# Kernel optimization log

Measured on AMD Instinct MI355X. Metric: run time of the kernel, lower is better.

Reference implementation:

```python
import jax, jax.numpy as jnp
import numpy as np

D_MODEL = 1024
D_STATE = 16
D_CONV = 4
EXPAND = 1
D_INNER = EXPAND * D_MODEL  # must equal D_MODEL for original dt_proj shapes to work
BATCH = 2
SEQ = 2048


def silu(x):
    return x * jax.nn.sigmoid(x)


def setup_inputs() -> dict:
    key = jax.random.key(0)
    ks = jax.random.split(key, 8)
    s = 0.02
    return {
        "x": jax.random.normal(ks[0], (BATCH, SEQ, D_MODEL), dtype=jnp.float32),
        "W_in": jax.random.normal(ks[1], (2 * D_INNER, D_MODEL), dtype=jnp.float32) * s,
        "conv_w": jax.random.normal(ks[2], (D_INNER, D_CONV), dtype=jnp.float32) * s,
        "conv_b": jnp.zeros((D_INNER,), dtype=jnp.float32),
        "W_dt": jax.random.normal(ks[3], (D_INNER, D_INNER), dtype=jnp.float32) * s,
        "b_dt": jnp.zeros((D_INNER,), dtype=jnp.float32),
        "A_log": jnp.zeros((D_INNER, D_STATE), dtype=jnp.float32),  # torch: log(ones)=0
        "Bp": jax.random.normal(ks[4], (D_INNER, D_STATE), dtype=jnp.float32),
        "Cp": jax.random.normal(ks[5], (D_INNER, D_STATE), dtype=jnp.float32),
        "Dp": jnp.ones((D_INNER,), dtype=jnp.float32),
        "W_out": jax.random.normal(ks[6], (D_MODEL, D_INNER), dtype=jnp.float32) * s,
    }


def reference(x, W_in, conv_w, conv_b, W_dt, b_dt, A_log, Bp, Cp, Dp, W_out):
    B, L, _ = x.shape
    # in_proj then split into ssm branch and gating residual
    xr = x @ W_in.T                               # (B, L, 2*D_INNER)
    x_proj, res = jnp.split(xr, 2, axis=-1)       # each (B, L, D_INNER)

    # causal depthwise conv1d (kernel D_CONV), == torch conv1d(padding=K-1)[..., :L]
    xp = jnp.pad(x_proj, ((0, 0), (D_CONV - 1, 0), (0, 0)))
    xc = conv_b + sum(conv_w[:, k] * xp[:, k:k + L, :] for k in range(D_CONV))
    xc = silu(xc)                                 # (B, L, D_INNER)

    # selective SSM scan
    delta = jax.nn.softplus(xc @ W_dt.T + b_dt)   # (B, L, D_INNER)
    A = -jnp.exp(A_log)                           # (D_INNER, D_STATE)
    dA = jnp.exp(delta[..., None] * A)            # (B, L, D_INNER, D_STATE)
    dBx = delta[..., None] * Bp * xc[..., None]   # (B, L, D_INNER, D_STATE)

    def step(h, inp):
        dA_t, dBx_t = inp                         # (B, D_INNER, D_STATE)
        h = dA_t * h + dBx_t
        y = jnp.einsum('bdn,dn->bd', h, Cp)
        return h, y

    h0 = jnp.zeros((B, D_INNER, D_STATE), dtype=x.dtype)
    _, ys = jax.lax.scan(step, h0, (dA.transpose(1, 0, 2, 3), dBx.transpose(1, 0, 2, 3)))
    x_ssm = ys.transpose(1, 0, 2) + xc * Dp       # (B, L, D_INNER)

    return (x_ssm * silu(res)) @ W_out.T          # (B, L, D_MODEL)
```

## Files before the change

### kernel.cpp

```cpp
#include <hip/hip_runtime.h>

typedef unsigned short u16;
typedef __bf16 bf16;
typedef bf16 bf16x8 __attribute__((ext_vector_type(8)));
typedef float f32x4 __attribute__((ext_vector_type(4)));

#define SEQ     2048
#define BATCH   2
#define DM      1024
#define DI      1024
#define NROW    (BATCH*SEQ)
#define NSTATE  16
#define NCHUNK  64
#define CLEN    32
#define BK      32

static_assert(SEQ == NCHUNK * CLEN, "chunking must cover SEQ");

__device__ __forceinline__ u16 f2bf(float f) {
  unsigned u = __builtin_bit_cast(unsigned, f);
  u += 0x7FFFu + ((u >> 16) & 1u);
  return (u16)(u >> 16);
}
__device__ __forceinline__ float sigm(float x) { return 1.f / (1.f + __expf(-x)); }

__global__ __launch_bounds__(256) void k_cvt_all(
    const float* __restrict__ x, const float* __restrict__ Win,
    const float* __restrict__ Wdt, const float* __restrict__ Wout,
    u16* __restrict__ xbf, u16* __restrict__ winbf,
    u16* __restrict__ wdtbf, u16* __restrict__ woutbf)
{
  long i = (long)blockIdx.x * 256 + threadIdx.x;
  const float* src; u16* dst; long off;
  if (i < 1048576)            { src = x;    dst = xbf;    off = i; }
  else if (i < 1572864)       { src = Win;  dst = winbf;  off = i - 1048576; }
  else if (i < 1835008)       { src = Wdt;  dst = wdtbf;  off = i - 1572864; }
  else                        { src = Wout; dst = woutbf; off = i - 1835008; }
  float4 v = reinterpret_cast<const float4*>(src)[off];
  ushort4 o;
  o.x = f2bf(v.x); o.y = f2bf(v.y); o.z = f2bf(v.z); o.w = f2bf(v.w);
  reinterpret_cast<ushort4*>(dst)[off] = o;
}


__device__ __forceinline__ void gload16(const u16* g, u16* l) {
  __builtin_amdgcn_global_load_lds((const __attribute__((address_space(1))) void*)g,
                                   (__attribute__((address_space(3))) void*)l,
                                   16, 0, 0);
}

template<int EPI, int BM, int BN, int GX>
__global__ __launch_bounds__(256, 4) void k_gemm(
    const u16* __restrict__ A, const u16* __restrict__ B,
    float* __restrict__ out0, float* __restrict__ out1,
    const float* __restrict__ bias, int M, int N, int K)
{
  constexpr int MI_ = BM / 32;
  constexpr int NI_ = BN / 32;
  __shared__ __align__(16) u16 sA[2 * BM * BK];
  __shared__ __align__(16) u16 sB[2 * BN * BK];
  const int t = threadIdx.x;
  const int wave = t >> 6, lane = t & 63;
  const int lr = lane & 15, kb = lane >> 4;
  const int wr = wave >> 1, wc = wave & 1;

  const int nwg = gridDim.x;
  const int bid = blockIdx.x;
  const int wg  = (bid & 7) * (nwg >> 3) + (bid >> 3);
  const long bm = (long)(wg / GX) * BM;
  const long bn = (long)(wg % GX) * BN;

  f32x4 acc[MI_][NI_] = {};

  const int srow = t >> 2;
  const int scol = (t & 3) * 8;
  const u16* gA0 = A + (bm + srow) * (long)K + scol;
  const u16* gB0 = B + (bn + srow) * (long)K + scol;

  auto STAGE = [&](int buf, int k0) {
    #pragma unroll
    for (int i = 0; i < BM / 64; ++i)
      gload16(gA0 + (long)i * 64 * K + k0,
              &sA[buf * (BM * BK) + i * (64 * BK) + wave * 512]);
    #pragma unroll
    for (int i = 0; i < BN / 64; ++i)
      gload16(gB0 + (long)i * 64 * K + k0,
              &sB[buf * (BN * BK) + i * (64 * BK) + wave * 512]);
  };

  STAGE(0, 0);
  __syncthreads();
  int cur = 0;
  for (int k0 = 0; k0 < K; k0 += BK) {
    if (k0 + BK < K) STAGE(cur ^ 1, k0 + BK);
    const u16* pa = &sA[cur * (BM * BK) + (wr * (BM / 2) + lr) * BK + kb * 8];
    const u16* pb = &sB[cur * (BN * BK) + (wc * (BN / 2) + lr) * BK + kb * 8];
    bf16x8 af[MI_], bfr[NI_];
    #pragma unroll
    for (int mi = 0; mi < MI_; ++mi)
      af[mi] = *reinterpret_cast<const bf16x8*>(pa + mi * 16 * BK);
    #pragma unroll
    for (int ni = 0; ni < NI_; ++ni)
      bfr[ni] = *reinterpret_cast<const bf16x8*>(pb + ni * 16 * BK);
    #pragma unroll
    for (int mi = 0; mi < MI_; ++mi)
      #pragma unroll
      for (int ni = 0; ni < NI_; ++ni)
        acc[mi][ni] = __builtin_amdgcn_mfma_f32_16x16x32_bf16(af[mi], bfr[ni], acc[mi][ni], 0, 0, 0);
    __syncthreads();
    cur ^= 1;
  }

  #pragma unroll
  for (int mi = 0; mi < MI_; ++mi) {
    const long row0 = bm + wr * (BM / 2) + mi * 16 + kb * 4;
    #pragma unroll
    for (int ni = 0; ni < NI_; ++ni) {
      const long col = bn + wc * (BN / 2) + ni * 16 + lr;
      #pragma unroll
      for (int j = 0; j < 4; ++j) {
        const float v = acc[mi][ni][j];
        const long r = row0 + j;
        if (EPI == 0) {
          out0[r * N + col] = v;
        } else if (EPI == 1) {
          if (col < DI) out0[r * DI + col] = v;
          else          out1[r * DI + (col - DI)] = v * sigm(v);
        } else {
          float z = v + bias[col];
          out0[r * N + col] = fmaxf(z, 0.f) + log1pf(__expf(-fabsf(z)));
        }
      }
    }
  }
}

__global__ void k_conv(const float* __restrict__ xproj, const float* __restrict__ convw,
                       const float* __restrict__ convb, float* __restrict__ xc,
                       u16* __restrict__ xcbf)
{
  const int idx = blockIdx.x * 256 + threadIdx.x;
  const int d = idx & (DI - 1);
  const int m = idx >> 10;
  const int l = m & (SEQ - 1);
  float acc = convb[d];
  #pragma unroll
  for (int k = 0; k < 4; ++k) {
    int ls = l + k - 3;
    if (ls >= 0)
      acc = fmaf(convw[d * 4 + k], xproj[(long)(m + k - 3) * DI + d], acc);
  }
  float s = acc * sigm(acc);
  xc[idx] = s;
  xcbf[idx] = f2bf(s);
}

__global__ __launch_bounds__(256) void k_scanA(
    const float* __restrict__ delta, const float* __restrict__ xc,
    const float* __restrict__ A_log, const float* __restrict__ Bp,
    float* __restrict__ hfin, float* __restrict__ sumdt_buf)
{
  const int tid = threadIdx.x, blk = blockIdx.x;
  const int d = (blk & 3) * 256 + tid;
  const int c = (blk >> 2) & (NCHUNK - 1);
  const int b = blk >> 8;
  float Aa[NSTATE], Bb[NSTATE], h[NSTATE];
  #pragma unroll
  for (int n = 0; n < NSTATE; ++n) {
    Aa[n] = -__expf(A_log[d * NSTATE + n]);
    Bb[n] = Bp[d * NSTATE + n];
    h[n] = 0.f;
  }
  const long base = ((long)(b * SEQ + c * CLEN)) * DI + d;
  float sdt = 0.f;
  for (int i = 0; i < CLEN; ++i) {
    float dt = delta[base + (long)i * DI];
    float x  = xc[base + (long)i * DI];
    sdt += dt;
    float dx = dt * x;
    #pragma unroll
    for (int n = 0; n < NSTATE; ++n) {
      float da = __expf(dt * Aa[n]);
      h[n] = fmaf(da, h[n], dx * Bb[n]);
    }
  }
  const long sb = ((long)(b * NCHUNK + c) * NSTATE) * DI + d;
  #pragma unroll
  for (int n = 0; n < NSTATE; ++n) hfin[sb + (long)n * DI] = h[n];
  sumdt_buf[(long)(b * NCHUNK + c) * DI + d] = sdt;
}

__global__ __launch_bounds__(256) void k_combine(
    const float* __restrict__ hfin, const float* __restrict__ sumdt_buf,
    const float* __restrict__ A_log, float* __restrict__ hstart)
{
  const int idx = blockIdx.x * 256 + threadIdx.x;
  const int d = idx & (DI - 1);
  const int n = (idx >> 10) & (NSTATE - 1);
  const int b = idx >> 14;
  const float Aa = -__expf(A_log[d * NSTATE + n]);
  float h = 0.f;
  for (int c = 0; c < NCHUNK; ++c) {
    const long sb = ((long)(b * NCHUNK + c) * NSTATE + n) * DI + d;
    hstart[sb] = h;
    float sdt = sumdt_buf[(long)(b * NCHUNK + c) * DI + d];
    h = fmaf(__expf(Aa * sdt), h, hfin[sb]);
  }
}

__global__ __launch_bounds__(256) void k_scanB(
    const float* __restrict__ delta, const float* __restrict__ xc,
    const float* __restrict__ A_log, const float* __restrict__ Bp,
    const float* __restrict__ Cp, const float* __restrict__ Dp,
    const float* __restrict__ sres, const float* __restrict__ hstart,
    u16* __restrict__ gated)
{
  const int tid = threadIdx.x, blk = blockIdx.x;
  const int d = (blk & 3) * 256 + tid;
  const int c = (blk >> 2) & (NCHUNK - 1);
  const int b = blk >> 8;
  float Aa[NSTATE], Bb[NSTATE], Cc[NSTATE], h[NSTATE];
  #pragma unroll
  for (int n = 0; n < NSTATE; ++n) {
    Aa[n] = -__expf(A_log[d * NSTATE + n]);
    Bb[n] = Bp[d * NSTATE + n];
    Cc[n] = Cp[d * NSTATE + n];
  }
  const float Dd = Dp[d];
  const long sb = ((long)(b * NCHUNK + c) * NSTATE) * DI + d;
  #pragma unroll
  for (int n = 0; n < NSTATE; ++n) h[n] = hstart[sb + (long)n * DI];
  const long base = ((long)(b * SEQ + c * CLEN)) * DI + d;
  for (int i = 0; i < CLEN; ++i) {
    float dt = delta[base + (long)i * DI];
    float x  = xc[base + (long)i * DI];
    float dx = dt * x;
    float y = 0.f;
    #pragma unroll
    for (int n = 0; n < NSTATE; ++n) {
      float da = __expf(dt * Aa[n]);
      h[n] = fmaf(da, h[n], dx * Bb[n]);
      y = fmaf(h[n], Cc[n], y);
    }
    float xs = fmaf(x, Dd, y);
    float g = xs * sres[base + (long)i * DI];
    gated[base + (long)i * DI] = f2bf(g);
  }
}

extern "C" void kernel_launch(void* const* d_in, const int* in_sizes, int n_in,
                              void* d_out, int out_size, void* d_ws, size_t ws_size,
                              hipStream_t stream)
{
  const float* x      = (const float*)d_in[0];
  const float* W_in   = (const float*)d_in[1];
  const float* conv_w = (const float*)d_in[2];
  const float* conv_b = (const float*)d_in[3];
  const float* W_dt   = (const float*)d_in[4];
  const float* b_dt   = (const float*)d_in[5];
  const float* A_log  = (const float*)d_in[6];
  const float* Bp     = (const float*)d_in[7];
  const float* Cp     = (const float*)d_in[8];
  const float* Dp     = (const float*)d_in[9];
  const float* W_out  = (const float*)d_in[10];
  float* out = (float*)d_out;

  const long MD = (long)NROW * DI;

  char* ws = (char*)d_ws;
  float* silu_res = (float*)ws;             ws += MD * 4;
  float* xc_f32   = (float*)ws;             ws += MD * 4;
  float* delta    = (float*)ws;             ws += MD * 4;
  u16*   xc_bf    = (u16*)ws;               ws += MD * 2;
  u16*   xbf      = (u16*)ws;               ws += MD * 2;
  u16*   Win_bf   = (u16*)ws;               ws += (long)2 * DI * DM * 2;
  u16*   Wdt_bf   = (u16*)ws;               ws += (long)DI * DI * 2;
  u16*   Wout_bf  = (u16*)ws;               ws += (long)DM * DI * 2;
  float* hfin     = (float*)ws;             ws += (long)BATCH * NCHUNK * NSTATE * DI * 4;
  float* sumdt    = (float*)ws;             ws += (long)BATCH * NCHUNK * DI * 4;
  float* hstart   = (float*)ws;             ws += (long)BATCH * NCHUNK * NSTATE * DI * 4;

  float* x_proj = delta;
  u16*   gated  = xbf;

  k_cvt_all<<<dim3(8192), dim3(256), 0, stream>>>(
      x, W_in, W_dt, W_out, xbf, Win_bf, Wdt_bf, Wout_bf);

  k_gemm<1, 128, 64, 32><<<dim3(1024), dim3(256), 0, stream>>>(
      xbf, Win_bf, x_proj, silu_res, nullptr, NROW, 2 * DI, DM);

  k_conv<<<dim3((unsigned)(MD / 256)), dim3(256), 0, stream>>>(x_proj, conv_w, conv_b, xc_f32, xc_bf);

  k_gemm<2, 64, 64, 16><<<dim3(1024), dim3(256), 0, stream>>>(
      xc_bf, Wdt_bf, delta, nullptr, b_dt, NROW, DI, DI);

  k_scanA<<<dim3(BATCH * NCHUNK * (DI / 256)), dim3(256), 0, stream>>>(
      delta, xc_f32, A_log, Bp, hfin, sumdt);
  k_combine<<<dim3(BATCH * NSTATE * DI / 256), dim3(256), 0, stream>>>(
      hfin, sumdt, A_log, hstart);
  k_scanB<<<dim3(BATCH * NCHUNK * (DI / 256)), dim3(256), 0, stream>>>(
      delta, xc_f32, A_log, Bp, Cp, Dp, silu_res, hstart, gated);

  k_gemm<0, 64, 64, 16><<<dim3(1024), dim3(256), 0, stream>>>(
      gated, Wout_bf, out, nullptr, nullptr, NROW, DM, DI);
}
```

Before: 168.2 us.

## Store intermediates in bf16 and widen GEMM K-tile with XOR-swizzled LDS

The silu(res), delta and xc intermediates are now stored as bf16 instead of fp32, and the scan kernels read them back as bf16. The goal is to roughly halve the memory traffic between the in-proj GEMM, the dt GEMM and the two scan passes, and the separate fp32 xc buffer goes away. Separately, the GEMM K-tile doubles from 32 to 64, and LDS columns are XOR-swizzled on both the global-to-LDS write and the fragment read, to cut bank conflicts and barrier count per K. In exchange the scan inputs carry bf16 rounding and LDS use per block doubles, which may lower occupancy.

```diff
diff --git a/kernel.cpp b/kernel.cpp
--- a/kernel.cpp
+++ b/kernel.cpp
@@ -13,7 +13,7 @@
 #define NSTATE  16
 #define NCHUNK  64
 #define CLEN    32
-#define BK      32
+#define BK      64
 
 static_assert(SEQ == NCHUNK * CLEN, "chunking must cover SEQ");
 
@@ -21,6 +21,9 @@
   unsigned u = __builtin_bit_cast(unsigned, f);
   u += 0x7FFFu + ((u >> 16) & 1u);
   return (u16)(u >> 16);
+}
+__device__ __forceinline__ float bf2f(u16 u) {
+  return __builtin_bit_cast(float, (unsigned)u << 16);
 }
 __device__ __forceinline__ float sigm(float x) { return 1.f / (1.f + __expf(-x)); }
 
@@ -52,7 +55,7 @@
 template<int EPI, int BM, int BN, int GX>
 __global__ __launch_bounds__(256, 4) void k_gemm(
     const u16* __restrict__ A, const u16* __restrict__ B,
-    float* __restrict__ out0, float* __restrict__ out1,
+    float* __restrict__ outf, u16* __restrict__ outb,
     const float* __restrict__ bias, int M, int N, int K)
 {
   constexpr int MI_ = BM / 32;
@@ -72,41 +75,51 @@
 
   f32x4 acc[MI_][NI_] = {};
 
-  const int srow = t >> 2;
-  const int scol = (t & 3) * 8;
-  const u16* gA0 = A + (bm + srow) * (long)K + scol;
-  const u16* gB0 = B + (bn + srow) * (long)K + scol;
+  const int srow = t >> 3;
+  const int gslot8 = (((t & 7) ^ (srow & 7)) * 8);
+  const u16* gA0 = A + (bm + srow) * (long)K + gslot8;
+  const u16* gB0 = B + (bn + srow) * (long)K + gslot8;
 
   auto STAGE = [&](int buf, int k0) {
     #pragma unroll
-    for (int i = 0; i < BM / 64; ++i)
-      gload16(gA0 + (long)i * 64 * K + k0,
-              &sA[buf * (BM * BK) + i * (64 * BK) + wave * 512]);
-    #pragma unroll
-    for (int i = 0; i < BN / 64; ++i)
-      gload16(gB0 + (long)i * 64 * K + k0,
-              &sB[buf * (BN * BK) + i * (64 * BK) + wave * 512]);
+    for (int i = 0; i < BM / 32; ++i)
+      gload16(gA0 + (long)i * 32 * K + k0,
+              &sA[buf * (BM * BK) + i * 2048 + wave * 512]);
+    #pragma unroll
+    for (int i = 0; i < BN / 32; ++i)
+      gload16(gB0 + (long)i * 32 * K + k0,
+              &sB[buf * (BN * BK) + i * 2048 + wave * 512]);
   };
 
+  const int xr8 = (lr & 7) * 8;
   STAGE(0, 0);
   __syncthreads();
   int cur = 0;
   for (int k0 = 0; k0 < K; k0 += BK) {
     if (k0 + BK < K) STAGE(cur ^ 1, k0 + BK);
-    const u16* pa = &sA[cur * (BM * BK) + (wr * (BM / 2) + lr) * BK + kb * 8];
-    const u16* pb = &sB[cur * (BN * BK) + (wc * (BN / 2) + lr) * BK + kb * 8];
-    bf16x8 af[MI_], bfr[NI_];
-    #pragma unroll
-    for (int mi = 0; mi < MI_; ++mi)
-      af[mi] = *reinterpret_cast<const bf16x8*>(pa + mi * 16 * BK);
-    #pragma unroll
-    for (int ni = 0; ni < NI_; ++ni)
-      bfr[ni] = *reinterpret_cast<const bf16x8*>(pb + ni * 16 * BK);
-    #pragma unroll
-    for (int mi = 0; mi < MI_; ++mi)
+    const u16* pa = &sA[cur * (BM * BK)];
+    const u16* pb = &sB[cur * (BN * BK)];
+    bf16x8 af[2][MI_], bfr[2][NI_];
+    #pragma unroll
+    for (int kk = 0; kk < 2; ++kk) {
+      const int co = ((kb * 8 + kk * 32) ^ xr8);
+      #pragma unroll
+      for (int mi = 0; mi < MI_; ++mi)
+        af[kk][mi] = *reinterpret_cast<const bf16x8*>(
+            pa + (wr * (BM / 2) + mi * 16 + lr) * BK + co);
       #pragma unroll
       for (int ni = 0; ni < NI_; ++ni)
-        acc[mi][ni] = __builtin_amdgcn_mfma_f32_16x16x32_bf16(af[mi], bfr[ni], acc[mi][ni], 0, 0, 0);
+        bfr[kk][ni] = *reinterpret_cast<const bf16x8*>(
+            pb + (wc * (BN / 2) + ni * 16 + lr) * BK + co);
+    }
+    #pragma unroll
+    for (int kk = 0; kk < 2; ++kk)
+      #pragma unroll
+      for (int mi = 0; mi < MI_; ++mi)
+        #pragma unroll
+        for (int ni = 0; ni < NI_; ++ni)
+          acc[mi][ni] = __builtin_amdgcn_mfma_f32_16x16x32_bf16(
+              af[kk][mi], bfr[kk][ni], acc[mi][ni], 0, 0, 0);
     __syncthreads();
     cur ^= 1;
   }
@@ -122,13 +135,13 @@
         const float v = acc[mi][ni][j];
         const long r = row0 + j;
         if (EPI == 0) {
-          out0[r * N + col] = v;
+          outf[r * N + col] = v;
         } else if (EPI == 1) {
-          if (col < DI) out0[r * DI + col] = v;
-          else          out1[r * DI + (col - DI)] = v * sigm(v);
+          if (col < DI) outf[r * DI + col] = v;
+          else          outb[r * DI + (col - DI)] = f2bf(v * sigm(v));
         } else {
           float z = v + bias[col];
-          out0[r * N + col] = fmaxf(z, 0.f) + log1pf(__expf(-fabsf(z)));
+          outb[r * N + col] = f2bf(fmaxf(z, 0.f) + log1pf(__expf(-fabsf(z))));
         }
       }
     }
@@ -136,8 +149,7 @@
 }
 
 __global__ void k_conv(const float* __restrict__ xproj, const float* __restrict__ convw,
-                       const float* __restrict__ convb, float* __restrict__ xc,
-                       u16* __restrict__ xcbf)
+                       const float* __restrict__ convb, u16* __restrict__ xcbf)
 {
   const int idx = blockIdx.x * 256 + threadIdx.x;
   const int d = idx & (DI - 1);
@@ -151,12 +163,11 @@
       acc = fmaf(convw[d * 4 + k], xproj[(long)(m + k - 3) * DI + d], acc);
   }
   float s = acc * sigm(acc);
-  xc[idx] = s;
   xcbf[idx] = f2bf(s);
 }
 
 __global__ __launch_bounds__(256) void k_scanA(
-    const float* __restrict__ delta, const float* __restrict__ xc,
+    const u16* __restrict__ delta, const u16* __restrict__ xc,
     const float* __restrict__ A_log, const float* __restrict__ Bp,
     float* __restrict__ hfin, float* __restrict__ sumdt_buf)
 {
@@ -174,8 +185,8 @@
   const long base = ((long)(b * SEQ + c * CLEN)) * DI + d;
   float sdt = 0.f;
   for (int i = 0; i < CLEN; ++i) {
-    float dt = delta[base + (long)i * DI];
-    float x  = xc[base + (long)i * DI];
+    float dt = bf2f(delta[base + (long)i * DI]);
+    float x  = bf2f(xc[base + (long)i * DI]);
     sdt += dt;
     float dx = dt * x;
     #pragma unroll
@@ -209,10 +220,10 @@
 }
 
 __global__ __launch_bounds__(256) void k_scanB(
-    const float* __restrict__ delta, const float* __restrict__ xc,
+    const u16* __restrict__ delta, const u16* __restrict__ xc,
     const float* __restrict__ A_log, const float* __restrict__ Bp,
     const float* __restrict__ Cp, const float* __restrict__ Dp,
-    const float* __restrict__ sres, const float* __restrict__ hstart,
+    const u16* __restrict__ sres, const float* __restrict__ hstart,
     u16* __restrict__ gated)
 {
   const int tid = threadIdx.x, blk = blockIdx.x;
@@ -232,8 +243,8 @@
   for (int n = 0; n < NSTATE; ++n) h[n] = hstart[sb + (long)n * DI];
   const long base = ((long)(b * SEQ + c * CLEN)) * DI + d;
   for (int i = 0; i < CLEN; ++i) {
-    float dt = delta[base + (long)i * DI];
-    float x  = xc[base + (long)i * DI];
+    float dt = bf2f(delta[base + (long)i * DI]);
+    float x  = bf2f(xc[base + (long)i * DI]);
     float dx = dt * x;
     float y = 0.f;
     #pragma unroll
@@ -243,7 +254,7 @@
       y = fmaf(h[n], Cc[n], y);
     }
     float xs = fmaf(x, Dd, y);
-    float g = xs * sres[base + (long)i * DI];
+    float g = xs * bf2f(sres[base + (long)i * DI]);
     gated[base + (long)i * DI] = f2bf(g);
   }
 }
@@ -268,9 +279,9 @@
   const long MD = (long)NROW * DI;
 
   char* ws = (char*)d_ws;
-  float* silu_res = (float*)ws;             ws += MD * 4;
-  float* xc_f32   = (float*)ws;             ws += MD * 4;
-  float* delta    = (float*)ws;             ws += MD * 4;
+  float* x_proj   = (float*)ws;             ws += MD * 4;
+  u16*   silu_bf  = (u16*)ws;               ws += MD * 2;
+  u16*   delta_bf = (u16*)ws;               ws += MD * 2;
   u16*   xc_bf    = (u16*)ws;               ws += MD * 2;
   u16*   xbf      = (u16*)ws;               ws += MD * 2;
   u16*   Win_bf   = (u16*)ws;               ws += (long)2 * DI * DM * 2;
@@ -280,26 +291,26 @@
   float* sumdt    = (float*)ws;             ws += (long)BATCH * NCHUNK * DI * 4;
   float* hstart   = (float*)ws;             ws += (long)BATCH * NCHUNK * NSTATE * DI * 4;
 
-  float* x_proj = delta;
-  u16*   gated  = xbf;
+  u16* gated = xbf;
 
   k_cvt_all<<<dim3(8192), dim3(256), 0, stream>>>(
       x, W_in, W_dt, W_out, xbf, Win_bf, Wdt_bf, Wout_bf);
 
   k_gemm<1, 128, 64, 32><<<dim3(1024), dim3(256), 0, stream>>>(
-      xbf, Win_bf, x_proj, silu_res, nullptr, NROW, 2 * DI, DM);
-
-  k_conv<<<dim3((unsigned)(MD / 256)), dim3(256), 0, stream>>>(x_proj, conv_w, conv_b, xc_f32, xc_bf);
+      xbf, Win_bf, x_proj, silu_bf, nullptr, NROW, 2 * DI, DM);
+
+  k_conv<<<dim3((unsigned)(MD / 256)), dim3(256), 0, stream>>>(
+      x_proj, conv_w, conv_b, xc_bf);
 
   k_gemm<2, 64, 64, 16><<<dim3(1024), dim3(256), 0, stream>>>(
-      xc_bf, Wdt_bf, delta, nullptr, b_dt, NROW, DI, DI);
+      xc_bf, Wdt_bf, nullptr, delta_bf, b_dt, NROW, DI, DI);
 
   k_scanA<<<dim3(BATCH * NCHUNK * (DI / 256)), dim3(256), 0, stream>>>(
-      delta, xc_f32, A_log, Bp, hfin, sumdt);
+      delta_bf, xc_bf, A_log, Bp, hfin, sumdt);
   k_combine<<<dim3(BATCH * NSTATE * DI / 256), dim3(256), 0, stream>>>(
       hfin, sumdt, A_log, hstart);
   k_scanB<<<dim3(BATCH * NCHUNK * (DI / 256)), dim3(256), 0, stream>>>(
-      delta, xc_f32, A_log, Bp, Cp, Dp, silu_res, hstart, gated);
+      delta_bf, xc_bf, A_log, Bp, Cp, Dp, silu_bf, hstart, gated);
 
   k_gemm<0, 64, 64, 16><<<dim3(1024), dim3(256), 0, stream>>>(
       gated, Wout_bf, out, nullptr, nullptr, NROW, DM, DI);
```

Measured after the change: 161.9 us. 3.8% less time.
